# Kernel optimization log

Measured on AMD Instinct MI355X. Metric: run time of the kernel, lower is better.

The kernel has to match this reference:

```python
import jax, jax.numpy as jnp
import numpy as np

WS = 16       # window size
SHIFT = 8     # shift size
HEADS = 16
DIM = 512
HIDDEN = 2048
B, H, W = 8, 64, 64
EPS = 1e-5


def _rel_coords_table(ws):
    h = np.arange(-(ws - 1), ws, dtype=np.float32)
    t = np.stack(np.meshgrid(h, h, indexing='ij'), axis=-1)  # (2ws-1, 2ws-1, 2)
    t = t / (ws - 1) * 8.0
    t = np.sign(t) * np.log2(np.abs(t) + 1.0) / np.log2(8.0)
    return t.reshape(-1, 2)


def _rel_pos_index(ws):
    coords = np.stack(np.meshgrid(np.arange(ws), np.arange(ws), indexing='ij'))
    cf = coords.reshape(2, -1)                      # (2, N)
    rel = (cf[:, :, None] - cf[:, None, :]).transpose(1, 2, 0)  # (N, N, 2)
    rel[..., 0] += ws - 1
    rel[..., 1] += ws - 1
    rel[..., 0] *= 2 * ws - 1
    return rel.sum(-1)                              # (N, N)


def _attn_mask(h, w, ws, shift):
    img = np.zeros((h, w))
    cnt = 0
    for hs in (slice(0, -ws), slice(-ws, -shift), slice(-shift, None)):
        for wsl in (slice(0, -ws), slice(-ws, -shift), slice(-shift, None)):
            img[hs, wsl] = cnt
            cnt += 1
    mw = img.reshape(h // ws, ws, w // ws, ws).transpose(0, 2, 1, 3).reshape(-1, ws * ws)
    am = mw[:, None, :] - mw[:, :, None]            # (nW, N, N)
    return np.where(am != 0, -100.0, 0.0).astype(np.float32)


def _ln(x, g, b):
    m = x.mean(-1, keepdims=True)
    v = ((x - m) ** 2).mean(-1, keepdims=True)
    return (x - m) * jax.lax.rsqrt(v + EPS) * g + b


def setup_inputs() -> dict:
    key = jax.random.key(0)
    ks = jax.random.split(key, 16)
    s = 0.02
    return {
        'x': jax.random.normal(ks[0], (B, H, W, DIM), jnp.float32),
        'qkv_w': jax.random.normal(ks[1], (3 * DIM, DIM), jnp.float32) * s,
        'q_bias': jnp.zeros((DIM,), jnp.float32),
        'v_bias': jnp.zeros((DIM,), jnp.float32),
        'logit_scale': jnp.full((HEADS, 1, 1), np.log(10.0), jnp.float32),
        'cpb_w1': jax.random.normal(ks[2], (512, 2), jnp.float32) * s,
        'cpb_b1': jnp.zeros((512,), jnp.float32),
        'cpb_w2': jax.random.normal(ks[3], (HEADS, 512), jnp.float32) * s,
        'proj_w': jax.random.normal(ks[4], (DIM, DIM), jnp.float32) * s,
        'proj_b': jnp.zeros((DIM,), jnp.float32),
        'norm1_g': jnp.ones((DIM,), jnp.float32),
        'norm1_b': jnp.zeros((DIM,), jnp.float32),
        'norm2_g': jnp.ones((DIM,), jnp.float32),
        'norm2_b': jnp.zeros((DIM,), jnp.float32),
        'fc1_w': jax.random.normal(ks[5], (HIDDEN, DIM), jnp.float32) * s,
        'fc1_b': jnp.zeros((HIDDEN,), jnp.float32),
        'fc2_w': jax.random.normal(ks[6], (DIM, HIDDEN), jnp.float32) * s,
        'fc2_b': jnp.zeros((DIM,), jnp.float32),
    }


def reference(x, qkv_w, q_bias, v_bias, logit_scale, cpb_w1, cpb_b1, cpb_w2,
              proj_w, proj_b, norm1_g, norm1_b, norm2_g, norm2_b,
              fc1_w, fc1_b, fc2_w, fc2_b):
    b, h, w, c = x.shape
    N = WS * WS
    nW = (h // WS) * (w // WS)
    hd = c // HEADS

    # --- shifted window cosine attention ---
    shifted = jnp.roll(x, (-SHIFT, -SHIFT), axis=(1, 2))
    xw = shifted.reshape(b, h // WS, WS, w // WS, WS, c)
    xw = xw.transpose(0, 1, 3, 2, 4, 5).reshape(-1, N, c)  # (b*nW, N, C)

    bias = jnp.concatenate([q_bias, jnp.zeros_like(q_bias), v_bias])
    qkv = (xw @ qkv_w.T + bias).reshape(-1, N, 3, HEADS, hd).transpose(2, 0, 3, 1, 4)
    q, k, v = qkv[0], qkv[1], qkv[2]  # (Bn, heads, N, hd)

    qn = q / jnp.maximum(jnp.linalg.norm(q, axis=-1, keepdims=True), 1e-12)
    kn = k / jnp.maximum(jnp.linalg.norm(k, axis=-1, keepdims=True), 1e-12)
    scale = jnp.exp(jnp.minimum(logit_scale, jnp.log(jnp.float32(100.0))))  # (heads,1,1)
    attn = jnp.einsum('bhnd,bhmd->bhnm', qn, kn) * scale

    # continuous relative position bias (CPB MLP)
    table = jnp.asarray(_rel_coords_table(WS))                    # (M, 2)
    t = jax.nn.relu(table @ cpb_w1.T + cpb_b1) @ cpb_w2.T          # (M, heads)
    idx = _rel_pos_index(WS).reshape(-1)
    rpb = t[idx].reshape(N, N, HEADS).transpose(2, 0, 1)
    rpb = 16.0 * jax.nn.sigmoid(rpb)
    attn = attn + rpb[None]

    mask = jnp.asarray(_attn_mask(h, w, WS, SHIFT))                # (nW, N, N)
    attn = attn.reshape(b, nW, HEADS, N, N) + mask[None, :, None]
    attn = jax.nn.softmax(attn.reshape(-1, HEADS, N, N), axis=-1)

    out = jnp.einsum('bhnm,bhmd->bhnd', attn, v).transpose(0, 2, 1, 3).reshape(-1, N, c)
    out = out @ proj_w.T + proj_b

    out = out.reshape(b, h // WS, w // WS, WS, WS, c)
    out = out.transpose(0, 1, 3, 2, 4, 5).reshape(b, h, w, c)
    out = jnp.roll(out, (SHIFT, SHIFT), axis=(1, 2))

    # post-norm residuals (SwinV2 style)
    x = x + _ln(out, norm1_g, norm1_b)
    hmid = jax.nn.gelu(x @ fc1_w.T + fc1_b, approximate=False)
    mlp_out = hmid @ fc2_w.T + fc2_b
    x = x + _ln(mlp_out, norm2_g, norm2_b)
    return x
```

## Files before the change

### kernel.cpp

```cpp
#include <hip/hip_runtime.h>
#include <math.h>


#define HEADS 16
#define HD 32
#define NTOK 256
#define DIMC 512
#define HIDDEN 2048

typedef __attribute__((ext_vector_type(8))) short bf16x8;
typedef __attribute__((ext_vector_type(4))) float f32x4;
typedef __attribute__((ext_vector_type(8))) unsigned short ushort8;

#define MFMA16(a, b, c) __builtin_amdgcn_mfma_f32_16x16x32_bf16((a), (b), (c), 0, 0, 0)
#define WAIT_VM(N) asm volatile("s_waitcnt vmcnt(" #N ")" ::: "memory")
#define WAIT_LGKM0 asm volatile("s_waitcnt lgkmcnt(0)" ::: "memory")

__device__ __forceinline__ unsigned short f2bf(float f) {
  union { float f; unsigned u; } v; v.f = f;
  unsigned r = v.u + 0x7FFFu + ((v.u >> 16) & 1u);
  return (unsigned short)(r >> 16);
}
__device__ __forceinline__ float bf2f(unsigned short h) {
  union { unsigned u; float f; } v; v.u = ((unsigned)h) << 16; return v.f;
}
__device__ __forceinline__ void gload16(const void* g, void* l) {
  __builtin_amdgcn_global_load_lds(
      (const __attribute__((address_space(1))) unsigned int*)g,
      (__attribute__((address_space(3))) unsigned int*)l, 16, 0, 0);
}
__device__ __forceinline__ bf16x8 ds_read128(const unsigned short* p) {
  unsigned off = (unsigned)(size_t)(const __attribute__((address_space(3))) unsigned short*)p;
  bf16x8 r;
  asm volatile("ds_read_b128 %0, %1" : "=v"(r) : "v"(off));
  return r;
}
__device__ __forceinline__ int band(int x) { return x < 48 ? 0 : (x < 56 ? 1 : 2); }

__device__ __forceinline__ float gelu_fast(float x) {
  float u2 = x * (1.5957691216f + 0.0713548163f * x * x);
  u2 = fminf(u2, 80.f);
  float e = __expf(u2);
  return x * (e / (e + 1.f));
}

__device__ __forceinline__ void gemm256_main(const unsigned short* Ab, const unsigned short* Bb,
                                             int K, unsigned short* aT, unsigned short* bT,
                                             f32x4 (&acc)[4][4]) {
  const int tid = threadIdx.x;
  const int w = tid >> 6, lane = tid & 63;
  const int cl = lane & 15, g = lane >> 4;
  const int wr = (w >> 2) * 64, wc = (w & 3) * 64;
  const int off0 = w * 1024 + lane * 16;
  const int r0 = off0 >> 6, c0 = ((off0 >> 4) & 3) ^ ((r0 >> 1) & 3);
  const char* Ac = (const char*)Ab;
  const char* Bc = (const char*)Bb;
  const size_t sA0 = (size_t)r0 * (K * 2) + (size_t)c0 * 16;
  const int T = K >> 5;
  int offB[4], offA0[4];
#pragma unroll
  for (int i = 0; i < 4; i++) {
    int rowb = wc + i * 16 + cl;
    offB[i] = rowb * 32 + ((g ^ ((rowb >> 1) & 3)) * 8);
    int rowa = wr + i * 16 + cl;
    offA0[i] = rowa * 32 + ((g ^ ((rowa >> 1) & 3)) * 8);
  }
#pragma unroll
  for (int p = 0; p < 3; p++) {
    size_t kb = (size_t)p * 64;
    int bo = p * 16384;
    gload16(Ac + sA0 + kb, (char*)aT + bo + off0);
    gload16(Bc + sA0 + kb, (char*)bT + bo + off0);
  }
  WAIT_VM(4);
  __builtin_amdgcn_s_barrier();
  bf16x8 bfv[4], af[4];
#pragma unroll
  for (int ni = 0; ni < 4; ni++) bfv[ni] = ds_read128(bT + offB[ni]);
#pragma unroll
  for (int mi = 0; mi < 4; mi++) af[mi] = ds_read128(aT + offA0[mi]);

  for (int t = 0; t < T; t++) {
    if (t + 3 < T) {
      size_t kb = (size_t)(t + 3) * 64;
      int bo = ((t + 3) & 3) * 16384;
      gload16(Ac + sA0 + kb, (char*)aT + bo + off0);
      gload16(Bc + sA0 + kb, (char*)bT + bo + off0);
    }
    WAIT_LGKM0;
    __builtin_amdgcn_sched_barrier(0);
    __builtin_amdgcn_s_setprio(1);
#pragma unroll
    for (int mi = 0; mi < 4; mi++)
#pragma unroll
      for (int ni = 0; ni < 4; ni++) acc[mi][ni] = MFMA16(af[mi], bfv[ni], acc[mi][ni]);
    __builtin_amdgcn_s_setprio(0);
    if (t + 1 < T) {
      if (t + 3 < T) WAIT_VM(4);
      else if (t + 2 < T) WAIT_VM(2);
      else WAIT_VM(0);
      __builtin_amdgcn_s_barrier();
      const int nxt = ((t + 1) & 3) * 8192;
#pragma unroll
      for (int ni = 0; ni < 4; ni++) bfv[ni] = ds_read128(bT + nxt + offB[ni]);
#pragma unroll
      for (int mi = 0; mi < 4; mi++) af[mi] = ds_read128(aT + nxt + offA0[mi]);
    }
  }
}

__device__ __forceinline__ void xcd_swizzle(int& bm, int& bn) {
  int gy = gridDim.y;
  int nwg = gridDim.x * gy;
  int flat = blockIdx.y * gridDim.x + blockIdx.x;
  int cpx = nwg >> 3;
  int swz = (flat & 7) * cpx + (flat >> 3);
  bm = swz / gy;
  bn = swz % gy;
}

__global__ __launch_bounds__(1024, 4) void gemm_qkv(const unsigned short* A,
                                                    const unsigned short* Bw, const float* qbias,
                                                    const float* vbias, unsigned short* qo,
                                                    unsigned short* ko, unsigned short* vo) {
  __shared__ unsigned short aT[4 * 8192];
  __shared__ unsigned short bT[4 * 8192];
  int bm, bn;
  xcd_swizzle(bm, bn);
  f32x4 acc[4][4] = {};
  gemm256_main(A + (size_t)bm * 256 * DIMC, Bw + (size_t)bn * 256 * DIMC, DIMC, aT, bT, acc);
  int lane = threadIdx.x & 63, w = threadIdx.x >> 6;
  int wr = (w >> 2) * 64, wc = (w & 3) * 64, g = lane >> 4, cl = lane & 15;
  int which = bn >> 1;
  unsigned short* base = which == 0 ? qo : (which == 1 ? ko : vo);
  float bvv[4];
  int headv[4], hdv[4];
#pragma unroll
  for (int ni = 0; ni < 4; ni++) {
    int gn = bn * 256 + wc + ni * 16 + cl;
    int wn = gn & 511;
    headv[ni] = wn >> 5;
    hdv[ni] = wn & 31;
    bvv[ni] = (which == 0) ? qbias[wn] : (which == 2 ? vbias[wn] : 0.f);
  }
#pragma unroll
  for (int mi = 0; mi < 4; mi++) {
#pragma unroll
    for (int reg = 0; reg < 4; reg++) {
      int gm = bm * 256 + wr + mi * 16 + 4 * g + reg;
      int win = gm >> 8, tok = gm & 255;
      float v0 = acc[mi][0][reg] + bvv[0];
      float v1 = acc[mi][1][reg] + bvv[1];
      float v2 = acc[mi][2][reg] + bvv[2];
      float v3 = acc[mi][3][reg] + bvv[3];
      if (which <= 1) {
        float sA = v0 * v0 + v1 * v1;
        float sB = v2 * v2 + v3 * v3;
#pragma unroll
        for (int m = 1; m < 16; m <<= 1) {
          sA += __shfl_xor(sA, m, 64);
          sB += __shfl_xor(sB, m, 64);
        }
        float rA = rsqrtf(fmaxf(sA, 1e-24f));
        float rB = rsqrtf(fmaxf(sB, 1e-24f));
        v0 *= rA; v1 *= rA; v2 *= rB; v3 *= rB;
      }
      size_t rowb = ((size_t)(win * HEADS)) * NTOK * HD + (size_t)tok * HD;
      base[rowb + (size_t)headv[0] * NTOK * HD + hdv[0]] = f2bf(v0);
      base[rowb + (size_t)headv[1] * NTOK * HD + hdv[1]] = f2bf(v1);
      base[rowb + (size_t)headv[2] * NTOK * HD + hdv[2]] = f2bf(v2);
      base[rowb + (size_t)headv[3] * NTOK * HD + hdv[3]] = f2bf(v3);
    }
  }
}

template <int GELU>
__global__ __launch_bounds__(1024, 4) void gemm_epi(const unsigned short* A,
                                                    const unsigned short* Bw, const float* bias,
                                                    unsigned short* out, int N, int K) {
  __shared__ unsigned short aT[4 * 8192];
  __shared__ unsigned short bT[4 * 8192];
  int bm, bn;
  xcd_swizzle(bm, bn);
  f32x4 acc[4][4] = {};
  gemm256_main(A + (size_t)bm * 256 * K, Bw + (size_t)bn * 256 * K, K, aT, bT, acc);
  int lane = threadIdx.x & 63, w = threadIdx.x >> 6;
  int wr = (w >> 2) * 64, wc = (w & 3) * 64, g = lane >> 4, cl = lane & 15;
  float bv[4];
#pragma unroll
  for (int ni = 0; ni < 4; ni++) bv[ni] = bias[bn * 256 + wc + ni * 16 + cl];
#pragma unroll
  for (int mi = 0; mi < 4; mi++) {
#pragma unroll
    for (int reg = 0; reg < 4; reg++) {
      int gm = bm * 256 + wr + mi * 16 + 4 * g + reg;
      unsigned short* rowp = out + (size_t)gm * N + bn * 256 + wc + cl;
#pragma unroll
      for (int ni = 0; ni < 4; ni++) {
        float val = acc[mi][ni][reg] + bv[ni];
        if (GELU) val = gelu_fast(val);
        rowp[ni * 16] = f2bf(val);
      }
    }
  }
}

__global__ __launch_bounds__(256) void attn_kernel(const unsigned short* qg,
                                                   const unsigned short* kg,
                                                   const unsigned short* vg, const float* rpbt,
                                                   const float* logit_scale,
                                                   unsigned short* attn_out) {
  __shared__ unsigned short kS[256 * 32];
  __shared__ unsigned short vT[32 * 256];
  __shared__ unsigned short pS[64 * 256];
  __shared__ float rpbS[961];

  int bid = blockIdx.x;
  int qb = bid & 3, h = (bid >> 2) & 15, win = bid >> 6;
  int tid = threadIdx.x, lane = tid & 63, w = tid >> 6;
  int g = lane >> 4, cl = lane & 15;
  const size_t whbase = ((size_t)(win * HEADS + h)) * NTOK * HD;
  const unsigned short* qwin = qg + whbase + (size_t)qb * 64 * HD;
  const unsigned short* kwin = kg + whbase;
  const unsigned short* vwin = vg + whbase;

#pragma unroll
  for (int i = 0; i < 4; i++) {
    int ci = i * 256 + tid, row = ci >> 2, gc = ci & 3;
    uint4 d = *(const uint4*)(kwin + row * 32 + gc * 8);
    *(uint4*)(kS + row * 32 + ((gc ^ ((row >> 1) & 3)) * 8)) = d;
  }
  {
    int tok = tid;
    ushort8 t0 = *(const ushort8*)(vwin + tok * 32);
    ushort8 t1 = *(const ushort8*)(vwin + tok * 32 + 8);
    ushort8 t2 = *(const ushort8*)(vwin + tok * 32 + 16);
    ushort8 t3 = *(const ushort8*)(vwin + tok * 32 + 24);
    int kc = tok >> 3, ki = tok & 7;
#pragma unroll
    for (int j = 0; j < 8; j++) {
      vT[(j)*256 + ((kc ^ (j & 7)) << 3) + ki] = t0[j];
      vT[(8 + j) * 256 + ((kc ^ ((8 + j) & 7)) << 3) + ki] = t1[j];
      vT[(16 + j) * 256 + ((kc ^ ((16 + j) & 7)) << 3) + ki] = t2[j];
      vT[(24 + j) * 256 + ((kc ^ ((24 + j) & 7)) << 3) + ki] = t3[j];
    }
  }
  for (int i = tid; i < 961; i += 256) rpbS[i] = rpbt[h * 961 + i];

  float scale = __expf(fminf(logit_scale[h], 4.6051702f));

  bf16x8 qf;
  {
    int qrow = 16 * w + cl;
    ushort8 qraw = *(const ushort8*)(qwin + qrow * 32 + 8 * g);
#pragma unroll
    for (int j = 0; j < 8; j++) qf[j] = (short)f2bf(bf2f(qraw[j]) * scale);
  }
  __syncthreads();

  f32x4 acc[16];
#pragma unroll
  for (int ct = 0; ct < 16; ct++) {
    int kr = ct * 16 + cl;
    bf16x8 kf = *(const bf16x8*)(kS + kr * 32 + ((g ^ ((kr >> 1) & 3)) * 8));
    f32x4 z = {0.f, 0.f, 0.f, 0.f};
    acc[ct] = MFMA16(qf, kf, z);
  }

  int wh = (win >> 2) & 3, ww = win & 3;
  int bandcc = band(ww * 16 + cl);
  const float C = scale + 16.f;
  int baseidx[4], ridq[4];
#pragma unroll
  for (int reg = 0; reg < 4; reg++) {
    int qrow = qb * 64 + 16 * w + 4 * g + reg;
    int ri = qrow >> 4, ci = qrow & 15;
    ridq[reg] = 3 * band(wh * 16 + ri) + band(ww * 16 + ci);
    baseidx[reg] = (ri + 15) * 31 + (ci + 15 - cl);
  }
  float s4[4] = {0.f, 0.f, 0.f, 0.f};
#pragma unroll
  for (int ct = 0; ct < 16; ct++) {
    int brc = 3 * band(wh * 16 + ct);
#pragma unroll
    for (int reg = 0; reg < 4; reg++) {
      float v = acc[ct][reg] + rpbS[baseidx[reg] - ct * 31] +
                ((ridq[reg] != (brc + bandcc)) ? -100.f : 0.f);
      float p = __expf(v - C);
      s4[reg] += p;
      int row = 16 * w + 4 * g + reg;
      int c = ct * 16 + cl;
      pS[row * 256 + (((c >> 3) ^ (row & 7)) << 3) + (c & 7)] = f2bf(p);
    }
  }
#pragma unroll
  for (int reg = 0; reg < 4; reg++) {
#pragma unroll
    for (int o = 1; o < 16; o <<= 1) s4[reg] += __shfl_xor(s4[reg], o, 64);
  }

  f32x4 o0 = {0.f, 0.f, 0.f, 0.f}, o1 = {0.f, 0.f, 0.f, 0.f};
  int prow = 16 * w + cl;
#pragma unroll
  for (int ks = 0; ks < 8; ks++) {
    bf16x8 pf = *(const bf16x8*)(pS + prow * 256 + ((((ks * 4 + g)) ^ (prow & 7)) << 3));
    int kc = ks * 4 + g;
    bf16x8 vf0 = *(const bf16x8*)(vT + cl * 256 + ((kc ^ (cl & 7)) << 3));
    bf16x8 vf1 = *(const bf16x8*)(vT + (16 + cl) * 256 + ((kc ^ ((16 + cl) & 7)) << 3));
    o0 = MFMA16(pf, vf0, o0);
    o1 = MFMA16(pf, vf1, o1);
  }

#pragma unroll
  for (int reg = 0; reg < 4; reg++) {
    int row = 16 * w + 4 * g + reg;
    float linv = 1.f / s4[reg];
    size_t tokg = (size_t)win * NTOK + qb * 64 + row;
    attn_out[tokg * DIMC + h * 32 + cl] = f2bf(o0[reg] * linv);
    attn_out[tokg * DIMC + h * 32 + 16 + cl] = f2bf(o1[reg] * linv);
  }
}

__global__ __launch_bounds__(256) void cvt_bf16(const float* src, unsigned short* dst, int n8) {
  int i = blockIdx.x * 256 + threadIdx.x;
  if (i >= n8) return;
  const float* s = src + (size_t)i * 8;
  float4 a = *(const float4*)s, b = *(const float4*)(s + 4);
  ushort8 o;
  o[0] = f2bf(a.x); o[1] = f2bf(a.y); o[2] = f2bf(a.z); o[3] = f2bf(a.w);
  o[4] = f2bf(b.x); o[5] = f2bf(b.y); o[6] = f2bf(b.z); o[7] = f2bf(b.w);
  *(ushort8*)(dst + (size_t)i * 8) = o;
}

__device__ __forceinline__ float cpb_coord(int i) {
  float t = (float)(i - 15) * (8.f / 15.f);
  float s = (t > 0.f) ? 1.f : ((t < 0.f) ? -1.f : 0.f);
  return s * log2f(fabsf(t) + 1.f) * (1.f / 3.f);
}

__global__ __launch_bounds__(256) void cpb_kernel(const float* w1, const float* b1, const float* w2,
                                                  float* rpbt) {
  int i = blockIdx.x * 256 + threadIdx.x;
  if (i >= 961 * 16) return;
  int m = i >> 4, h = i & 15;
  int mi = m / 31, mj = m % 31;
  float c0 = cpb_coord(mi), c1 = cpb_coord(mj);
  float acc = 0.f;
  for (int j = 0; j < 512; j++) {
    float hv = fmaxf(w1[2 * j] * c0 + w1[2 * j + 1] * c1 + b1[j], 0.f);
    acc += hv * w2[h * 512 + j];
  }
  rpbt[h * 961 + m] = 16.f / (1.f + __expf(-acc));
}

__global__ __launch_bounds__(256) void xw_gather(const float* x, unsigned short* xw) {
  int idx = blockIdx.x * 256 + threadIdx.x;
  int m = idx >> 6, chunk = idx & 63;
  int win = m >> 8, tok = m & 255;
  int b = win >> 4, wh = (win >> 2) & 3, ww = win & 3;
  int tr = tok >> 4, tc = tok & 15;
  int sr = (wh * 16 + tr + 8) & 63, sc = (ww * 16 + tc + 8) & 63;
  const float* src = x + ((size_t)((b * 64 + sr) * 64 + sc)) * 512 + chunk * 8;
  float4 a = *(const float4*)src, bq = *(const float4*)(src + 4);
  ushort8 o;
  o[0] = f2bf(a.x); o[1] = f2bf(a.y); o[2] = f2bf(a.z); o[3] = f2bf(a.w);
  o[4] = f2bf(bq.x); o[5] = f2bf(bq.y); o[6] = f2bf(bq.z); o[7] = f2bf(bq.w);
  *(ushort8*)(xw + (size_t)m * 512 + chunk * 8) = o;
}

__global__ __launch_bounds__(256) void ln1_kernel(const unsigned short* pr, const float* x,
                                                  const float* gw, const float* bw,
                                                  unsigned short* x1b) {
  int w = threadIdx.x >> 6, lane = threadIdx.x & 63;
  size_t t = (size_t)blockIdx.x * 4 + w;
  int ti = (int)t;
  int b = ti >> 12, rc = ti & 4095, r = rc >> 6, c = rc & 63;
  int sr = (r + 56) & 63, sc = (c + 56) & 63;
  int win = b * 16 + (sr >> 4) * 4 + (sc >> 4);
  int tok = (sr & 15) * 16 + (sc & 15);
  int ch = lane * 8;
  ushort8 pv = *(const ushort8*)(pr + ((size_t)win * 256 + tok) * 512 + ch);
  float pf[8];
  float s = 0.f, s2 = 0.f;
#pragma unroll
  for (int j = 0; j < 8; j++) { pf[j] = bf2f(pv[j]); s += pf[j]; s2 += pf[j] * pf[j]; }
#pragma unroll
  for (int o = 1; o < 64; o <<= 1) { s += __shfl_xor(s, o, 64); s2 += __shfl_xor(s2, o, 64); }
  float mean = s * (1.f / 512.f);
  float rstd = rsqrtf(s2 * (1.f / 512.f) - mean * mean + 1e-5f);
  const float* xrow = x + t * 512 + ch;
  float4 xa = *(const float4*)xrow, xb = *(const float4*)(xrow + 4);
  float xs[8] = {xa.x, xa.y, xa.z, xa.w, xb.x, xb.y, xb.z, xb.w};
  ushort8 o8;
#pragma unroll
  for (int j = 0; j < 8; j++) {
    float y = (pf[j] - mean) * rstd * gw[ch + j] + bw[ch + j];
    o8[j] = f2bf(xs[j] + y);
  }
  *(ushort8*)(x1b + t * 512 + ch) = o8;
}

__global__ __launch_bounds__(256) void ln2_kernel(const unsigned short* mp,
                                                  const unsigned short* x1b, const float* gw,
                                                  const float* bw, float* out) {
  int w = threadIdx.x >> 6, lane = threadIdx.x & 63;
  size_t t = (size_t)blockIdx.x * 4 + w;
  int ch = lane * 8;
  ushort8 mv = *(const ushort8*)(mp + t * 512 + ch);
  float pf[8];
  float s = 0.f, s2 = 0.f;
#pragma unroll
  for (int j = 0; j < 8; j++) { pf[j] = bf2f(mv[j]); s += pf[j]; s2 += pf[j] * pf[j]; }
#pragma unroll
  for (int o = 1; o < 64; o <<= 1) { s += __shfl_xor(s, o, 64); s2 += __shfl_xor(s2, o, 64); }
  float mean = s * (1.f / 512.f);
  float rstd = rsqrtf(s2 * (1.f / 512.f) - mean * mean + 1e-5f);
  ushort8 xv = *(const ushort8*)(x1b + t * 512 + ch);
  float vals[8];
#pragma unroll
  for (int j = 0; j < 8; j++)
    vals[j] = bf2f(xv[j]) + (pf[j] - mean) * rstd * gw[ch + j] + bw[ch + j];
  *(float4*)(out + t * 512 + ch) = make_float4(vals[0], vals[1], vals[2], vals[3]);
  *(float4*)(out + t * 512 + ch + 4) = make_float4(vals[4], vals[5], vals[6], vals[7]);
}

extern "C" void kernel_launch(void* const* d_in, const int* in_sizes, int n_in, void* d_out,
                              int out_size, void* d_ws, size_t ws_size, hipStream_t stream) {
  (void)in_sizes; (void)n_in; (void)out_size; (void)ws_size;
  const float* x = (const float*)d_in[0];
  const float* qkv_w = (const float*)d_in[1];
  const float* q_bias = (const float*)d_in[2];
  const float* v_bias = (const float*)d_in[3];
  const float* logit_sc = (const float*)d_in[4];
  const float* cpb_w1 = (const float*)d_in[5];
  const float* cpb_b1 = (const float*)d_in[6];
  const float* cpb_w2 = (const float*)d_in[7];
  const float* proj_w = (const float*)d_in[8];
  const float* proj_b = (const float*)d_in[9];
  const float* n1g = (const float*)d_in[10];
  const float* n1b = (const float*)d_in[11];
  const float* n2g = (const float*)d_in[12];
  const float* n2b = (const float*)d_in[13];
  const float* fc1_w = (const float*)d_in[14];
  const float* fc1_b = (const float*)d_in[15];
  const float* fc2_w = (const float*)d_in[16];
  const float* fc2_b = (const float*)d_in[17];

  char* ws = (char*)d_ws;
  unsigned short* wq = (unsigned short*)(ws);
  unsigned short* wp = (unsigned short*)(ws + (2ll << 20));
  unsigned short* w1 = (unsigned short*)(ws + (4ll << 20));
  unsigned short* w2 = (unsigned short*)(ws + (8ll << 20));
  float* rpbt = (float*)(ws + (12ll << 20));
  unsigned short* xw = (unsigned short*)(ws + (16ll << 20));
  unsigned short* qbuf = (unsigned short*)(ws + (48ll << 20));
  unsigned short* kbuf = (unsigned short*)(ws + (80ll << 20));
  unsigned short* vbuf = (unsigned short*)(ws + (112ll << 20));
  unsigned short* projout = (unsigned short*)(ws + (144ll << 20));
  unsigned short* x1b = (unsigned short*)(ws + (176ll << 20));
  unsigned short* hmid = (unsigned short*)(ws + (48ll << 20));
  unsigned short* mlpout = xw;
  float* out = (float*)d_out;

  cvt_bf16<<<dim3(384), dim3(256), 0, stream>>>(qkv_w, wq, 1536 * 512 / 8);
  cvt_bf16<<<dim3(128), dim3(256), 0, stream>>>(proj_w, wp, 512 * 512 / 8);
  cvt_bf16<<<dim3(512), dim3(256), 0, stream>>>(fc1_w, w1, 2048 * 512 / 8);
  cvt_bf16<<<dim3(512), dim3(256), 0, stream>>>(fc2_w, w2, 512 * 2048 / 8);
  cpb_kernel<<<dim3(61), dim3(256), 0, stream>>>(cpb_w1, cpb_b1, cpb_w2, rpbt);
  xw_gather<<<dim3(8192), dim3(256), 0, stream>>>(x, xw);

  gemm_qkv<<<dim3(128, 6), dim3(1024), 0, stream>>>(xw, wq, q_bias, v_bias, qbuf, kbuf, vbuf);
  attn_kernel<<<dim3(8192), dim3(256), 0, stream>>>(qbuf, kbuf, vbuf, rpbt, logit_sc, xw);
  gemm_epi<0><<<dim3(128, 2), dim3(1024), 0, stream>>>(xw, wp, proj_b, projout, 512, 512);
  ln1_kernel<<<dim3(8192), dim3(256), 0, stream>>>(projout, x, n1g, n1b, x1b);

  gemm_epi<1><<<dim3(128, 8), dim3(1024), 0, stream>>>(x1b, w1, fc1_b, hmid, 2048, 512);
  gemm_epi<0><<<dim3(128, 2), dim3(1024), 0, stream>>>(hmid, w2, fc2_b, mlpout, 512, 2048);
  ln2_kernel<<<dim3(8192), dim3(256), 0, stream>>>(mlpout, x1b, n2g, n2b, out);
}
```

Baseline: 485.0 us.

## Use 4-wave 256x256 GEMM tiles with 128x128 per-wave register blocking

The 256x256 block GEMM now runs with 256 threads (4 waves) instead of 1024, and each wave computes a 128x128 sub-tile with an 8x8 accumulator array. LDS fragments are reused across more MFMAs, which cuts LDS read traffic per flop, and the per-k-step loop is restructured into two MFMA half-passes with the barrier moved to the loop top. The trade is far higher VGPR/AGPR pressure (256 accumulator floats per lane), so only one block fits per CU and fewer waves are available to hide latency, with a risk of register spills.

Result: slower. 553.7 us (+14.2%).

```diff
diff --git a/kernel.cpp b/kernel.cpp
--- a/kernel.cpp
+++ b/kernel.cpp
@@ -46,66 +46,80 @@
 
 __device__ __forceinline__ void gemm256_main(const unsigned short* Ab, const unsigned short* Bb,
                                              int K, unsigned short* aT, unsigned short* bT,
-                                             f32x4 (&acc)[4][4]) {
+                                             f32x4 (&acc)[8][8]) {
   const int tid = threadIdx.x;
   const int w = tid >> 6, lane = tid & 63;
   const int cl = lane & 15, g = lane >> 4;
-  const int wr = (w >> 2) * 64, wc = (w & 3) * 64;
-  const int off0 = w * 1024 + lane * 16;
-  const int r0 = off0 >> 6, c0 = ((off0 >> 4) & 3) ^ ((r0 >> 1) & 3);
+  const int wr = (w >> 1) * 128, wc = (w & 1) * 128;
   const char* Ac = (const char*)Ab;
   const char* Bc = (const char*)Bb;
-  const size_t sA0 = (size_t)r0 * (K * 2) + (size_t)c0 * 16;
-  const int T = K >> 5;
-  int offB[4], offA0[4];
+  size_t sAs[4];
+  int offs[4];
 #pragma unroll
   for (int i = 0; i < 4; i++) {
+    int off = w * 4096 + i * 1024 + lane * 16;
+    offs[i] = off;
+    int r = off >> 6, c = ((off >> 4) & 3) ^ ((r >> 1) & 3);
+    sAs[i] = (size_t)r * (K * 2) + (size_t)c * 16;
+  }
+  int offA[8], offB[8];
+#pragma unroll
+  for (int i = 0; i < 8; i++) {
+    int rowa = wr + i * 16 + cl;
+    offA[i] = rowa * 32 + ((g ^ ((rowa >> 1) & 3)) * 8);
     int rowb = wc + i * 16 + cl;
     offB[i] = rowb * 32 + ((g ^ ((rowb >> 1) & 3)) * 8);
-    int rowa = wr + i * 16 + cl;
-    offA0[i] = rowa * 32 + ((g ^ ((rowa >> 1) & 3)) * 8);
-  }
+  }
+  const int T = K >> 5;
 #pragma unroll
   for (int p = 0; p < 3; p++) {
     size_t kb = (size_t)p * 64;
     int bo = p * 16384;
-    gload16(Ac + sA0 + kb, (char*)aT + bo + off0);
-    gload16(Bc + sA0 + kb, (char*)bT + bo + off0);
-  }
-  WAIT_VM(4);
-  __builtin_amdgcn_s_barrier();
-  bf16x8 bfv[4], af[4];
-#pragma unroll
-  for (int ni = 0; ni < 4; ni++) bfv[ni] = ds_read128(bT + offB[ni]);
-#pragma unroll
-  for (int mi = 0; mi < 4; mi++) af[mi] = ds_read128(aT + offA0[mi]);
-
+#pragma unroll
+    for (int i = 0; i < 4; i++) {
+      gload16(Ac + sAs[i] + kb, (char*)aT + bo + offs[i]);
+      gload16(Bc + sAs[i] + kb, (char*)bT + bo + offs[i]);
+    }
+  }
   for (int t = 0; t < T; t++) {
+    if (t + 2 < T) WAIT_VM(16);
+    else if (t + 1 < T) WAIT_VM(8);
+    else WAIT_VM(0);
+    __builtin_amdgcn_s_barrier();
     if (t + 3 < T) {
       size_t kb = (size_t)(t + 3) * 64;
       int bo = ((t + 3) & 3) * 16384;
-      gload16(Ac + sA0 + kb, (char*)aT + bo + off0);
-      gload16(Bc + sA0 + kb, (char*)bT + bo + off0);
-    }
+#pragma unroll
+      for (int i = 0; i < 4; i++) {
+        gload16(Ac + sAs[i] + kb, (char*)aT + bo + offs[i]);
+        gload16(Bc + sAs[i] + kb, (char*)bT + bo + offs[i]);
+      }
+    }
+    const int cur = (t & 3) * 8192;
+    bf16x8 fB[8], fA[4];
+#pragma unroll
+    for (int ni = 0; ni < 8; ni++) fB[ni] = ds_read128(bT + cur + offB[ni]);
+#pragma unroll
+    for (int mi = 0; mi < 4; mi++) fA[mi] = ds_read128(aT + cur + offA[mi]);
     WAIT_LGKM0;
     __builtin_amdgcn_sched_barrier(0);
     __builtin_amdgcn_s_setprio(1);
 #pragma unroll
     for (int mi = 0; mi < 4; mi++)
 #pragma unroll
-      for (int ni = 0; ni < 4; ni++) acc[mi][ni] = MFMA16(af[mi], bfv[ni], acc[mi][ni]);
+      for (int ni = 0; ni < 8; ni++) acc[mi][ni] = MFMA16(fA[mi], fB[ni], acc[mi][ni]);
     __builtin_amdgcn_s_setprio(0);
-    if (t + 1 < T) {
-      if (t + 3 < T) WAIT_VM(4);
-      else if (t + 2 < T) WAIT_VM(2);
-      else WAIT_VM(0);
-      __builtin_amdgcn_s_barrier();
-      const int nxt = ((t + 1) & 3) * 8192;
-#pragma unroll
-      for (int ni = 0; ni < 4; ni++) bfv[ni] = ds_read128(bT + nxt + offB[ni]);
-#pragma unroll
-      for (int mi = 0; mi < 4; mi++) af[mi] = ds_read128(aT + nxt + offA0[mi]);
-    }
+    bf16x8 fA2[4];
+#pragma unroll
+    for (int mi = 0; mi < 4; mi++) fA2[mi] = ds_read128(aT + cur + offA[4 + mi]);
+    WAIT_LGKM0;
+    __builtin_amdgcn_sched_barrier(0);
+    __builtin_amdgcn_s_setprio(1);
+#pragma unroll
+    for (int mi = 0; mi < 4; mi++)
+#pragma unroll
+      for (int ni = 0; ni < 8; ni++) acc[4 + mi][ni] = MFMA16(fA2[mi], fB[ni], acc[4 + mi][ni]);
+    __builtin_amdgcn_s_setprio(0);
   }
 }
 
@@ -119,24 +133,24 @@
   bn = swz % gy;
 }
 
-__global__ __launch_bounds__(1024, 4) void gemm_qkv(const unsigned short* A,
-                                                    const unsigned short* Bw, const float* qbias,
-                                                    const float* vbias, unsigned short* qo,
-                                                    unsigned short* ko, unsigned short* vo) {
+__global__ __launch_bounds__(256, 1) void gemm_qkv(const unsigned short* A,
+                                                   const unsigned short* Bw, const float* qbias,
+                                                   const float* vbias, unsigned short* qo,
+                                                   unsigned short* ko, unsigned short* vo) {
   __shared__ unsigned short aT[4 * 8192];
   __shared__ unsigned short bT[4 * 8192];
   int bm, bn;
   xcd_swizzle(bm, bn);
-  f32x4 acc[4][4] = {};
+  f32x4 acc[8][8] = {};
   gemm256_main(A + (size_t)bm * 256 * DIMC, Bw + (size_t)bn * 256 * DIMC, DIMC, aT, bT, acc);
   int lane = threadIdx.x & 63, w = threadIdx.x >> 6;
-  int wr = (w >> 2) * 64, wc = (w & 3) * 64, g = lane >> 4, cl = lane & 15;
+  int wr = (w >> 1) * 128, wc = (w & 1) * 128, g = lane >> 4, cl = lane & 15;
   int which = bn >> 1;
   unsigned short* base = which == 0 ? qo : (which == 1 ? ko : vo);
-  float bvv[4];
-  int headv[4], hdv[4];
-#pragma unroll
-  for (int ni = 0; ni < 4; ni++) {
+  float bvv[8];
+  int headv[8], hdv[8];
+#pragma unroll
+  for (int ni = 0; ni < 8; ni++) {
     int gn = bn * 256 + wc + ni * 16 + cl;
     int wn = gn & 511;
     headv[ni] = wn >> 5;
@@ -144,59 +158,56 @@
     bvv[ni] = (which == 0) ? qbias[wn] : (which == 2 ? vbias[wn] : 0.f);
   }
 #pragma unroll
-  for (int mi = 0; mi < 4; mi++) {
+  for (int mi = 0; mi < 8; mi++) {
 #pragma unroll
     for (int reg = 0; reg < 4; reg++) {
       int gm = bm * 256 + wr + mi * 16 + 4 * g + reg;
       int win = gm >> 8, tok = gm & 255;
-      float v0 = acc[mi][0][reg] + bvv[0];
-      float v1 = acc[mi][1][reg] + bvv[1];
-      float v2 = acc[mi][2][reg] + bvv[2];
-      float v3 = acc[mi][3][reg] + bvv[3];
+      float v[8];
+#pragma unroll
+      for (int ni = 0; ni < 8; ni++) v[ni] = acc[mi][ni][reg] + bvv[ni];
       if (which <= 1) {
-        float sA = v0 * v0 + v1 * v1;
-        float sB = v2 * v2 + v3 * v3;
-#pragma unroll
-        for (int m = 1; m < 16; m <<= 1) {
-          sA += __shfl_xor(sA, m, 64);
-          sB += __shfl_xor(sB, m, 64);
+#pragma unroll
+        for (int p = 0; p < 4; p++) {
+          float s = v[2 * p] * v[2 * p] + v[2 * p + 1] * v[2 * p + 1];
+#pragma unroll
+          for (int m = 1; m < 16; m <<= 1) s += __shfl_xor(s, m, 64);
+          float r = rsqrtf(fmaxf(s, 1e-24f));
+          v[2 * p] *= r;
+          v[2 * p + 1] *= r;
         }
-        float rA = rsqrtf(fmaxf(sA, 1e-24f));
-        float rB = rsqrtf(fmaxf(sB, 1e-24f));
-        v0 *= rA; v1 *= rA; v2 *= rB; v3 *= rB;
       }
       size_t rowb = ((size_t)(win * HEADS)) * NTOK * HD + (size_t)tok * HD;
-      base[rowb + (size_t)headv[0] * NTOK * HD + hdv[0]] = f2bf(v0);
-      base[rowb + (size_t)headv[1] * NTOK * HD + hdv[1]] = f2bf(v1);
-      base[rowb + (size_t)headv[2] * NTOK * HD + hdv[2]] = f2bf(v2);
-      base[rowb + (size_t)headv[3] * NTOK * HD + hdv[3]] = f2bf(v3);
+#pragma unroll
+      for (int ni = 0; ni < 8; ni++)
+        base[rowb + (size_t)headv[ni] * NTOK * HD + hdv[ni]] = f2bf(v[ni]);
     }
   }
 }
 
 template <int GELU>
-__global__ __launch_bounds__(1024, 4) void gemm_epi(const unsigned short* A,
-                                                    const unsigned short* Bw, const float* bias,
-                                                    unsigned short* out, int N, int K) {
+__global__ __launch_bounds__(256, 1) void gemm_epi(const unsigned short* A,
+                                                   const unsigned short* Bw, const float* bias,
+                                                   unsigned short* out, int N, int K) {
   __shared__ unsigned short aT[4 * 8192];
   __shared__ unsigned short bT[4 * 8192];
   int bm, bn;
   xcd_swizzle(bm, bn);
-  f32x4 acc[4][4] = {};
+  f32x4 acc[8][8] = {};
   gemm256_main(A + (size_t)bm * 256 * K, Bw + (size_t)bn * 256 * K, K, aT, bT, acc);
   int lane = threadIdx.x & 63, w = threadIdx.x >> 6;
-  int wr = (w >> 2) * 64, wc = (w & 3) * 64, g = lane >> 4, cl = lane & 15;
-  float bv[4];
-#pragma unroll
-  for (int ni = 0; ni < 4; ni++) bv[ni] = bias[bn * 256 + wc + ni * 16 + cl];
-#pragma unroll
-  for (int mi = 0; mi < 4; mi++) {
+  int wr = (w >> 1) * 128, wc = (w & 1) * 128, g = lane >> 4, cl = lane & 15;
+  float bv[8];
+#pragma unroll
+  for (int ni = 0; ni < 8; ni++) bv[ni] = bias[bn * 256 + wc + ni * 16 + cl];
+#pragma unroll
+  for (int mi = 0; mi < 8; mi++) {
 #pragma unroll
     for (int reg = 0; reg < 4; reg++) {
       int gm = bm * 256 + wr + mi * 16 + 4 * g + reg;
       unsigned short* rowp = out + (size_t)gm * N + bn * 256 + wc + cl;
 #pragma unroll
-      for (int ni = 0; ni < 4; ni++) {
+      for (int ni = 0; ni < 8; ni++) {
         float val = acc[mi][ni][reg] + bv[ni];
         if (GELU) val = gelu_fast(val);
         rowp[ni * 16] = f2bf(val);
@@ -469,12 +480,12 @@
   cpb_kernel<<<dim3(61), dim3(256), 0, stream>>>(cpb_w1, cpb_b1, cpb_w2, rpbt);
   xw_gather<<<dim3(8192), dim3(256), 0, stream>>>(x, xw);
 
-  gemm_qkv<<<dim3(128, 6), dim3(1024), 0, stream>>>(xw, wq, q_bias, v_bias, qbuf, kbuf, vbuf);
+  gemm_qkv<<<dim3(128, 6), dim3(256), 0, stream>>>(xw, wq, q_bias, v_bias, qbuf, kbuf, vbuf);
   attn_kernel<<<dim3(8192), dim3(256), 0, stream>>>(qbuf, kbuf, vbuf, rpbt, logit_sc, xw);
-  gemm_epi<0><<<dim3(128, 2), dim3(1024), 0, stream>>>(xw, wp, proj_b, projout, 512, 512);
+  gemm_epi<0><<<dim3(128, 2), dim3(256), 0, stream>>>(xw, wp, proj_b, projout, 512, 512);
   ln1_kernel<<<dim3(8192), dim3(256), 0, stream>>>(projout, x, n1g, n1b, x1b);
 
-  gemm_epi<1><<<dim3(128, 8), dim3(1024), 0, stream>>>(x1b, w1, fc1_b, hmid, 2048, 512);
-  gemm_epi<0><<<dim3(128, 2), dim3(1024), 0, stream>>>(hmid, w2, fc2_b, mlpout, 512, 2048);
+  gemm_epi<1><<<dim3(128, 8), dim3(256), 0, stream>>>(x1b, w1, fc1_b, hmid, 2048, 512);
+  gemm_epi<0><<<dim3(128, 2), dim3(256), 0, stream>>>(hmid, w2, fc2_b, mlpout, 512, 2048);
   ln2_kernel<<<dim3(8192), dim3(256), 0, stream>>>(mlpout, x1b, n2g, n2b, out);
 }
```
